# Optimization experiments

Hardware: AMD Instinct MI355X
Metric: run time of the kernel (lower is better)

Reference implementation:

```python
import jax, jax.numpy as jnp
import numpy as np
import math

B, S, D, H = 4, 2048, 2048, 16
HD = D // H  # 128


def _alibi_slopes(n_heads):
    # standard ALiBi slopes: 2^(-8/n * (h+1))
    return jnp.asarray([2.0 ** (-8.0 / n_heads * (h + 1)) for h in range(n_heads)], dtype=jnp.float32)


def setup_inputs() -> dict:
    key = jax.random.key(0)
    ks = jax.random.split(key, 10)
    w = lambda k: jax.random.normal(k, (D, D), dtype=jnp.float32) * 0.02
    b = lambda k: jax.random.normal(k, (D,), dtype=jnp.float32) * 0.01
    return {
        "hidden_states": jax.random.normal(ks[0], (B, S, D), dtype=jnp.float32),
        "Wq": w(ks[1]), "bq": b(ks[2]),
        "Wk": w(ks[3]), "bk": b(ks[4]),
        "Wv": w(ks[5]), "bv": b(ks[6]),
        "Wo": w(ks[7]), "bo": b(ks[8]),
        "alibi_slopes": _alibi_slopes(H),
    }


def reference(hidden_states, Wq, bq, Wk, bk, Wv, bv, Wo, bo, alibi_slopes):
    Bn, t, _ = hidden_states.shape
    split = lambda x: x.reshape(Bn, t, H, HD).transpose(0, 2, 1, 3)  # [B,H,S,hd]
    q = split(hidden_states @ Wq.T + bq)
    k = split(hidden_states @ Wk.T + bk)
    v = split(hidden_states @ Wv.T + bv)

    scores = jnp.einsum("bhsd,bhtd->bhst", q, k)  # [B,H,S,S]
    pos = jnp.arange(t)
    # alibi bias added BEFORE the 1/sqrt(hd) scaling, as in the torch code
    rel = (pos[None, :] - pos[:, None]).astype(scores.dtype)  # j - i
    bias = alibi_slopes[:, None, None] * rel  # [H,S,S]
    scores = (scores + bias[None]) / math.sqrt(HD)
    # grok-style tanh rescaling
    scores = 30.0 * jnp.tanh(scores / 30.0)
    causal = pos[:, None] >= pos[None, :]  # [S,S]
    scores = jnp.where(causal[None, None], scores, -jnp.inf)
    probs = jax.nn.softmax(scores, axis=-1)
    ctx = jnp.einsum("bhst,bhtd->bhsd", probs, v)
    ctx = ctx.transpose(0, 2, 1, 3).reshape(Bn, t, D)
    return ctx @ Wo.T + bo
```

## Files before the change

### kernel.cpp

```cpp
#include <hip/hip_runtime.h>

typedef unsigned int u32;
typedef unsigned short u16;
typedef __bf16 bf16x8 __attribute__((ext_vector_type(8)));
typedef float f32x4 __attribute__((ext_vector_type(4)));


__device__ __forceinline__ u16 f2bf(float f) {
  u32 u = __builtin_bit_cast(u32, f);
  u32 r = u + 0x7fffu + ((u >> 16) & 1u);
  return (u16)(r >> 16);
}

__device__ __forceinline__ void gload_lds16(const void* g, void* l) {
  __builtin_amdgcn_global_load_lds(
      (__attribute__((address_space(1))) void*)(g),
      (__attribute__((address_space(3))) void*)(l), 16, 0, 0);
}


__global__ __launch_bounds__(256) void convert_kernel(
    const float* __restrict__ hs, const float* __restrict__ wq,
    const float* __restrict__ wk, const float* __restrict__ wv,
    const float* __restrict__ wo,
    u16* __restrict__ hsb, u16* __restrict__ wqb, u16* __restrict__ wkb,
    u16* __restrict__ wvb, u16* __restrict__ wob) {
  long t = (long)blockIdx.x * 256 + threadIdx.x;
  const float* src;
  u16* dst;
  long off;
  if (t < 2097152) {
    src = hs; dst = hsb; off = t << 3;
  } else {
    long u = t - 2097152;
    int wi = (int)(u >> 19);
    off = (u & 524287) << 3;
    if (wi == 0)      { src = wq; dst = wqb; }
    else if (wi == 1) { src = wk; dst = wkb; }
    else if (wi == 2) { src = wv; dst = wvb; }
    else              { src = wo; dst = wob; }
  }
  float4 a = *(const float4*)(src + off);
  float4 b = *(const float4*)(src + off + 4);
  uint4 o;
  o.x = (u32)f2bf(a.x) | ((u32)f2bf(a.y) << 16);
  o.y = (u32)f2bf(a.z) | ((u32)f2bf(a.w) << 16);
  o.z = (u32)f2bf(b.x) | ((u32)f2bf(b.y) << 16);
  o.w = (u32)f2bf(b.z) | ((u32)f2bf(b.w) << 16);
  *(uint4*)(dst + off) = o;
}


template <int OF32>
__global__ __launch_bounds__(512, 2) void gemm256_kernel(
    const u16* __restrict__ A, const u16* __restrict__ Bw,
    const float* __restrict__ bias0, const float* __restrict__ bias1,
    const float* __restrict__ bias2, void* __restrict__ o0,
    void* __restrict__ o1, void* __restrict__ o2, int m_tiles, int n_tiles) {
  __shared__ __align__(16) char L[2][2][2][16384];

  const int tid = threadIdx.x;
  const int lane = tid & 63, w = tid >> 6;
  const int lr = lane & 15, lk = lane >> 4;
  const int wm = (w >> 2) * 128, wn = (w & 3) * 64;

  const int bid = blockIdx.x;
  const int xcd = bid & 7, loc = bid >> 3;
  const int npx = n_tiles >> 3;
  const int n_idx = xcd * npx + loc % npx;
  const int m_idx = loc / npx;
  const int m0 = m_idx * 256, n0 = n_idx * 256;

  const char* Ab = (const char*)A;
  const char* Bb = (const char*)Bw;
  const char* gA[2];
  const char* gB[2];
#pragma unroll
  for (int j = 0; j < 2; j++) {
    const int o = j * 8192 + tid * 16;
    const int row = o >> 6;
    const int c = (o & 63) ^ (((row >> 1) & 3) << 4);
    gA[j] = Ab + (size_t)(m0 + row) * 4096 + c;
    gB[j] = Bb + (size_t)(n0 + row) * 4096 + c;
  }

  auto stage = [&](int t, int kh, int isB) {
    char* Ld = &L[t & 1][isB][kh][0] + tid * 16;
    const int gof = t * 128 + kh * 64;
#pragma unroll
    for (int j = 0; j < 2; j++)
      gload_lds16((isB ? gB[j] : gA[j]) + gof, Ld + j * 8192);
  };
  auto rdA = [&](bf16x8* dst, int buf, int kh, int mset) {
#pragma unroll
    for (int m = 0; m < 4; m++) {
      const int row = wm + mset * 64 + m * 16 + lr;
      const int c = (lk * 16) ^ (((row >> 1) & 3) << 4);
      dst[m] = *(const bf16x8*)(&L[buf][0][kh][0] + row * 64 + c);
    }
  };
  auto rdB = [&](bf16x8* dst, int buf, int kh) {
#pragma unroll
    for (int n = 0; n < 4; n++) {
      const int row = wn + n * 16 + lr;
      const int c = (lk * 16) ^ (((row >> 1) & 3) << 4);
      dst[n] = *(const bf16x8*)(&L[buf][1][kh][0] + row * 64 + c);
    }
  };

  f32x4 acc[2][4][4];
#pragma unroll
  for (int s = 0; s < 2; s++)
#pragma unroll
    for (int m = 0; m < 4; m++)
#pragma unroll
      for (int n = 0; n < 4; n++) acc[s][m][n] = {0.f, 0.f, 0.f, 0.f};

  auto mm = [&](f32x4 (&ac)[4][4], bf16x8* a_, bf16x8* b_) {
    __builtin_amdgcn_s_setprio(1);
#pragma unroll
    for (int m = 0; m < 4; m++)
#pragma unroll
      for (int n = 0; n < 4; n++)
        ac[m][n] = __builtin_amdgcn_mfma_f32_16x16x32_bf16(a_[m], b_[n],
                                                           ac[m][n], 0, 0, 0);
    __builtin_amdgcn_s_setprio(0);
  };

  stage(0, 0, 0); stage(0, 0, 1); stage(0, 1, 0); stage(0, 1, 1);

  bf16x8 aP[4], aQ[4], b0[4], b1[4];
  for (int t = 0; t < 32; ++t) {
    const int buf = t & 1;
    const int t1 = (t + 1 < 32) ? t + 1 : 31;
    asm volatile("s_waitcnt vmcnt(4)" ::: "memory");
    asm volatile("s_barrier" ::: "memory");
    rdA(aP, buf, 0, 0);
    rdB(b0, buf, 0);
    stage(t1, 0, 0);
    if (t) mm(acc[1], aQ, b1);
    rdA(aQ, buf, 0, 1);
    stage(t1, 0, 1);
    mm(acc[0], aP, b0);
    asm volatile("s_waitcnt vmcnt(4)" ::: "memory");
    asm volatile("s_barrier" ::: "memory");
    rdA(aP, buf, 1, 0);
    rdB(b1, buf, 1);
    stage(t1, 1, 0);
    mm(acc[1], aQ, b0);
    rdA(aQ, buf, 1, 1);
    stage(t1, 1, 1);
    mm(acc[0], aP, b1);
  }
  mm(acc[1], aQ, b1);

  const float* bias;
  void* op;
  int nl0;
  if (OF32) {
    bias = bias0; op = o0; nl0 = n0;
  } else {
    const int seg = n0 >> 11;
    bias = seg == 0 ? bias0 : (seg == 1 ? bias1 : bias2);
    op = seg == 0 ? o0 : (seg == 1 ? o1 : o2);
    nl0 = n0 & 2047;
  }
#pragma unroll
  for (int n = 0; n < 4; n++) {
    const int col = nl0 + wn + n * 16 + lr;
    const float bv = bias[col];
#pragma unroll
    for (int s = 0; s < 2; s++)
#pragma unroll
      for (int m = 0; m < 4; m++) {
        const int grow = m0 + wm + s * 64 + m * 16 + lk * 4;
#pragma unroll
        for (int r = 0; r < 4; r++) {
          const float v = acc[s][m][n][r] + bv;
          if (OF32)
            ((float*)op)[(size_t)(grow + r) * 2048 + col] = v;
          else
            ((u16*)op)[(size_t)(grow + r) * 2048 + col] = f2bf(v);
        }
      }
  }
}


__global__ __launch_bounds__(512, 2) void attn_kernel(
    const u16* __restrict__ Qm, const u16* __restrict__ Km,
    const u16* __restrict__ Vm, const float* __restrict__ slopes,
    u16* __restrict__ ctx) {
  __shared__ __align__(16) char Ks[64 * 256];
  __shared__ __align__(16) char Vt[2][128 * 128];
  __shared__ __align__(16) char Pb[8][16 * 128];

  const int bid = blockIdx.x;
  const int sw = (bid & 7) * 64 + (bid >> 3);
  const int bh = sw >> 3, pi = sw & 7;
  const int b = bh >> 4, h = bh & 15;
  const int NTA = 2 * pi + 2;

  const int tid = threadIdx.x;
  const int lane = tid & 63, w = tid >> 6;
  const int lr = lane & 15, lk = lane >> 4;

  const char* Qb = (const char*)Qm + (size_t)b * 2048 * 4096 + h * 256;
  const char* Kb = (const char*)Km + (size_t)b * 2048 * 4096 + h * 256;
  const char* Vb = (const char*)Vm + (size_t)b * 2048 * 4096 + h * 256;

  const float SCALE = 0.08838834764831845f;
  const float sl_c = slopes[h] * SCALE;

  const float C1 = 1.4426950408889634f;
  const float C3 = -5.343315e-4f;
  const float C5 = 2.374806e-7f;
  const float C7 = -1.068005e-10f;

  float Tt[16];
#pragma unroll
  for (int nb = 0; nb < 4; nb++)
#pragma unroll
    for (int r = 0; r < 4; r++) Tt[nb * 4 + r] = sl_c * (float)(nb * 16 - r);

  const int vd0 = (tid & 15) * 8;
  const int vkv2 = tid >> 4;

  uint4 vr0, vr1;

  auto kvt_of = [&](int it) { return it < NTA ? it : it - NTA; };

  auto stageK = [&](int it) {
    const int kv0 = kvt_of(it) * 64;
#pragma unroll
    for (int j = 0; j < 2; j++) {
      const int o = j * 8192 + tid * 16;
      const int row = o >> 8, c = (o & 255) ^ ((row & 7) << 4);
      gload_lds16(Kb + (size_t)(kv0 + row) * 4096 + c, Ks + o);
    }
  };
  auto loadV = [&](int it) {
    const int kv0 = kvt_of(it) * 64;
    vr0 = *(const uint4*)(Vb + (size_t)(kv0 + vkv2 * 2) * 4096 + vd0 * 2);
    vr1 = *(const uint4*)(Vb + (size_t)(kv0 + vkv2 * 2 + 1) * 4096 + vd0 * 2);
  };
  auto writeV = [&](int bufi) {
    const u32* p0 = (const u32*)&vr0;
    const u32* p1 = (const u32*)&vr1;
#pragma unroll
    for (int wd = 0; wd < 4; wd++) {
      const u32 ev = __builtin_amdgcn_perm(p1[wd], p0[wd], 0x05040100u);
      const u32 od = __builtin_amdgcn_perm(p1[wd], p0[wd], 0x07060302u);
      const int d0_ = vd0 + 2 * wd, d1_ = d0_ + 1;
      *(u32*)(Vt[bufi] + d0_ * 128 +
              ((vkv2 * 4) ^ (((d0_ ^ (d0_ >> 3)) & 7) << 4))) = ev;
      *(u32*)(Vt[bufi] + d1_ * 128 +
              ((vkv2 * 4) ^ (((d1_ ^ (d1_ >> 3)) & 7) << 4))) = od;
    }
  };

  bf16x8 qf[4];
  f32x4 pv[8];
  float rs[4];
  int q0 = 0;

  stageK(0);
  loadV(0);

  for (int it = 0; it < 34; ++it) {
    const int bufi = it & 1;
    const int kv0 = kvt_of(it) * 64;

    if (it == 0 || it == NTA) {
      const int st = (it == 0) ? pi : (15 - pi);
      q0 = st * 128 + w * 16;
#pragma unroll
      for (int kc = 0; kc < 4; kc++)
        qf[kc] =
            *(const bf16x8*)(Qb + (size_t)(q0 + lr) * 4096 + kc * 64 + lk * 16);
#pragma unroll
      for (int i = 0; i < 8; i++) pv[i] = {0.f, 0.f, 0.f, 0.f};
      rs[0] = rs[1] = rs[2] = rs[3] = 0.f;
    }

    writeV(bufi);
    asm volatile("s_waitcnt vmcnt(0)" ::: "memory");
    __syncthreads();

    if (it + 1 < 34) loadV(it + 1);

    f32x4 sc[4];
    __builtin_amdgcn_s_setprio(1);
#pragma unroll
    for (int nb = 0; nb < 4; nb++) {
      f32x4 a = {0.f, 0.f, 0.f, 0.f};
      const int krow = nb * 16 + lr;
#pragma unroll
      for (int kc = 0; kc < 4; kc++) {
        const int off = krow * 256 + ((kc * 64 + lk * 16) ^ ((krow & 7) << 4));
        bf16x8 kf = *(const bf16x8*)(Ks + off);
        a = __builtin_amdgcn_mfma_f32_16x16x32_bf16(qf[kc], kf, a, 0, 0, 0);
      }
      sc[nb] = a;
    }
    __builtin_amdgcn_s_setprio(0);

    __syncthreads();
    if (it + 1 < 34) stageK(it + 1);

    const float aliB = sl_c * (float)(kv0 + lr - q0 - lk * 4);
#pragma unroll
    for (int nb = 0; nb < 4; nb++) {
      const int kv = kv0 + nb * 16 + lr;
#pragma unroll
      for (int r = 0; r < 4; r++) {
        const int q = q0 + lk * 4 + r;
        float z = fmaf(sc[nb][r], SCALE, aliB + Tt[nb * 4 + r]);
        z = fmaxf(-16.0f, fminf(z, 16.0f));
        const float u2 = z * z;
        float hh = fmaf(u2, C7, C5);
        hh = fmaf(u2, hh, C3);
        hh = fmaf(u2, hh, C1);
        float p = exp2f(z * hh);
        p = (kv <= q) ? p : 0.0f;
        rs[r] += p;
        const int qq = lk * 4 + r;
        const int off = qq * 128 + (((nb * 16 + lr) * 2) ^ ((qq & 7) << 4));
        const u32 ub = __builtin_bit_cast(u32, p);
        *(u16*)(Pb[w] + off) = (u16)((ub + 0x8000u) >> 16);
      }
    }

    __builtin_amdgcn_s_setprio(1);
#pragma unroll
    for (int kc = 0; kc < 2; kc++) {
      const int poff = lr * 128 + ((kc * 64 + lk * 16) ^ ((lr & 7) << 4));
      bf16x8 pf = *(const bf16x8*)(Pb[w] + poff);
#pragma unroll
      for (int db = 0; db < 8; db++) {
        const int d = db * 16 + lr;
        const int voff =
            d * 128 + ((kc * 64 + lk * 16) ^ (((d ^ (d >> 3)) & 7) << 4));
        bf16x8 vf = *(const bf16x8*)(Vt[bufi] + voff);
        pv[db] = __builtin_amdgcn_mfma_f32_16x16x32_bf16(pf, vf, pv[db], 0, 0, 0);
      }
    }
    __builtin_amdgcn_s_setprio(0);

    if (it == NTA - 1 || it == 33) {
      float inv[4];
#pragma unroll
      for (int r = 0; r < 4; r++) {
        float s = rs[r];
        s += __shfl_xor(s, 1);
        s += __shfl_xor(s, 2);
        s += __shfl_xor(s, 4);
        s += __shfl_xor(s, 8);
        inv[r] = 1.0f / s;
      }
      const size_t baserow = (size_t)b * 2048 + q0 + lk * 4;
#pragma unroll
      for (int db = 0; db < 8; db++)
#pragma unroll
        for (int r = 0; r < 4; r++)
          ctx[(baserow + r) * 2048 + h * 128 + db * 16 + lr] =
              f2bf(pv[db][r] * inv[r]);
    }
  }
}


extern "C" void kernel_launch(void* const* d_in, const int* in_sizes, int n_in,
                              void* d_out, int out_size, void* d_ws,
                              size_t ws_size, hipStream_t stream) {
  const float* hs = (const float*)d_in[0];
  const float* Wq = (const float*)d_in[1];
  const float* bq = (const float*)d_in[2];
  const float* Wk = (const float*)d_in[3];
  const float* bk = (const float*)d_in[4];
  const float* Wv = (const float*)d_in[5];
  const float* bv = (const float*)d_in[6];
  const float* Wo = (const float*)d_in[7];
  const float* bo = (const float*)d_in[8];
  const float* slopes = (const float*)d_in[9];

  char* ws = (char*)d_ws;
  u16* hsb = (u16*)(ws);
  u16* wqb = (u16*)(ws + 33554432);
  u16* wkb = (u16*)(ws + 41943040);
  u16* wvb = (u16*)(ws + 50331648);
  u16* wob = (u16*)(ws + 58720256);
  u16* Qb  = (u16*)(ws + 67108864);
  u16* Kb  = (u16*)(ws + 100663296);
  u16* Vb  = (u16*)(ws + 134217728);
  u16* ctxb = hsb;

  convert_kernel<<<16384, 256, 0, stream>>>(hs, Wq, Wk, Wv, Wo, hsb, wqb, wkb,
                                            wvb, wob);
  gemm256_kernel<0><<<768, 512, 0, stream>>>(hsb, wqb, bq, bk, bv, Qb, Kb, Vb,
                                             32, 24);
  attn_kernel<<<512, 512, 0, stream>>>(Qb, Kb, Vb, slopes, ctxb);
  gemm256_kernel<1><<<256, 512, 0, stream>>>(ctxb, wob, bo, bo, bo, d_out,
                                             d_out, d_out, 32, 8);
}
```

Before: 477.0 us.

## Double-buffer K tiles in LDS, single-buffer V, skip causal mask off-diagonal

Moves double buffering from the transposed V tile to the K tile, so the next K tile's global-to-LDS load is issued right after the barrier and overlaps the QK^T and softmax work of the current iteration. The barrier that sat between QK^T and the K staging is removed, and a new barrier is placed before the V write to protect the single V buffer. The per-element ALiBi bias precompute is folded into one register table plus a scalar, clamping uses med3, and the causal mask compare now runs only on diagonal tiles. The exchange is a different barrier placement and a changed LDS footprint, which could affect occupancy at two blocks per CU.

```diff
diff --git a/kernel.cpp b/kernel.cpp
--- a/kernel.cpp
+++ b/kernel.cpp
@@ -191,8 +191,8 @@
     const u16* __restrict__ Qm, const u16* __restrict__ Km,
     const u16* __restrict__ Vm, const float* __restrict__ slopes,
     u16* __restrict__ ctx) {
-  __shared__ __align__(16) char Ks[64 * 256];
-  __shared__ __align__(16) char Vt[2][128 * 128];
+  __shared__ __align__(16) char Ks[2][64 * 256];
+  __shared__ __align__(16) char Vt[128 * 128];
   __shared__ __align__(16) char Pb[8][16 * 128];
 
   const int bid = blockIdx.x;
@@ -217,11 +217,12 @@
   const float C5 = 2.374806e-7f;
   const float C7 = -1.068005e-10f;
 
-  float Tt[16];
+  float zo[16];
 #pragma unroll
   for (int nb = 0; nb < 4; nb++)
 #pragma unroll
-    for (int r = 0; r < 4; r++) Tt[nb * 4 + r] = sl_c * (float)(nb * 16 - r);
+    for (int r = 0; r < 4; r++)
+      zo[nb * 4 + r] = sl_c * (float)((lr - lk * 4) + nb * 16 - r);
 
   const int vd0 = (tid & 15) * 8;
   const int vkv2 = tid >> 4;
@@ -230,13 +231,13 @@
 
   auto kvt_of = [&](int it) { return it < NTA ? it : it - NTA; };
 
-  auto stageK = [&](int it) {
+  auto stageK = [&](int it, int buf) {
     const int kv0 = kvt_of(it) * 64;
 #pragma unroll
     for (int j = 0; j < 2; j++) {
       const int o = j * 8192 + tid * 16;
       const int row = o >> 8, c = (o & 255) ^ ((row & 7) << 4);
-      gload_lds16(Kb + (size_t)(kv0 + row) * 4096 + c, Ks + o);
+      gload_lds16(Kb + (size_t)(kv0 + row) * 4096 + c, Ks[buf] + o);
     }
   };
   auto loadV = [&](int it) {
@@ -244,7 +245,7 @@
     vr0 = *(const uint4*)(Vb + (size_t)(kv0 + vkv2 * 2) * 4096 + vd0 * 2);
     vr1 = *(const uint4*)(Vb + (size_t)(kv0 + vkv2 * 2 + 1) * 4096 + vd0 * 2);
   };
-  auto writeV = [&](int bufi) {
+  auto writeV = [&]() {
     const u32* p0 = (const u32*)&vr0;
     const u32* p1 = (const u32*)&vr1;
 #pragma unroll
@@ -252,9 +253,9 @@
       const u32 ev = __builtin_amdgcn_perm(p1[wd], p0[wd], 0x05040100u);
       const u32 od = __builtin_amdgcn_perm(p1[wd], p0[wd], 0x07060302u);
       const int d0_ = vd0 + 2 * wd, d1_ = d0_ + 1;
-      *(u32*)(Vt[bufi] + d0_ * 128 +
+      *(u32*)(Vt + d0_ * 128 +
               ((vkv2 * 4) ^ (((d0_ ^ (d0_ >> 3)) & 7) << 4))) = ev;
-      *(u32*)(Vt[bufi] + d1_ * 128 +
+      *(u32*)(Vt + d1_ * 128 +
               ((vkv2 * 4) ^ (((d1_ ^ (d1_ >> 3)) & 7) << 4))) = od;
     }
   };
@@ -264,11 +265,11 @@
   float rs[4];
   int q0 = 0;
 
-  stageK(0);
+  stageK(0, 0);
   loadV(0);
 
   for (int it = 0; it < 34; ++it) {
-    const int bufi = it & 1;
+    const int kb = it & 1;
     const int kv0 = kvt_of(it) * 64;
 
     if (it == 0 || it == NTA) {
@@ -283,11 +284,15 @@
       rs[0] = rs[1] = rs[2] = rs[3] = 0.f;
     }
 
-    writeV(bufi);
+    __syncthreads();
+    writeV();
     asm volatile("s_waitcnt vmcnt(0)" ::: "memory");
     __syncthreads();
 
-    if (it + 1 < 34) loadV(it + 1);
+    if (it + 1 < 34) {
+      stageK(it + 1, kb ^ 1);
+      loadV(it + 1);
+    }
 
     f32x4 sc[4];
     __builtin_amdgcn_s_setprio(1);
@@ -298,31 +303,31 @@
 #pragma unroll
       for (int kc = 0; kc < 4; kc++) {
         const int off = krow * 256 + ((kc * 64 + lk * 16) ^ ((krow & 7) << 4));
-        bf16x8 kf = *(const bf16x8*)(Ks + off);
+        bf16x8 kf = *(const bf16x8*)(Ks[kb] + off);
         a = __builtin_amdgcn_mfma_f32_16x16x32_bf16(qf[kc], kf, a, 0, 0, 0);
       }
       sc[nb] = a;
     }
     __builtin_amdgcn_s_setprio(0);
 
-    __syncthreads();
-    if (it + 1 < 34) stageK(it + 1);
-
-    const float aliB = sl_c * (float)(kv0 + lr - q0 - lk * 4);
+    const bool diag = (it < NTA) ? (it >= NTA - 2) : (it >= 32);
+    const float sb = sl_c * (float)(kv0 - q0);
 #pragma unroll
     for (int nb = 0; nb < 4; nb++) {
-      const int kv = kv0 + nb * 16 + lr;
 #pragma unroll
       for (int r = 0; r < 4; r++) {
-        const int q = q0 + lk * 4 + r;
-        float z = fmaf(sc[nb][r], SCALE, aliB + Tt[nb * 4 + r]);
-        z = fmaxf(-16.0f, fminf(z, 16.0f));
+        float z = fmaf(sc[nb][r], SCALE, zo[nb * 4 + r] + sb);
+        z = __builtin_amdgcn_fmed3f(z, -16.0f, 16.0f);
         const float u2 = z * z;
         float hh = fmaf(u2, C7, C5);
         hh = fmaf(u2, hh, C3);
         hh = fmaf(u2, hh, C1);
         float p = exp2f(z * hh);
-        p = (kv <= q) ? p : 0.0f;
+        if (diag) {
+          const int kv = kv0 + nb * 16 + lr;
+          const int q = q0 + lk * 4 + r;
+          p = (kv <= q) ? p : 0.0f;
+        }
         rs[r] += p;
         const int qq = lk * 4 + r;
         const int off = qq * 128 + (((nb * 16 + lr) * 2) ^ ((qq & 7) << 4));
@@ -341,7 +346,7 @@
         const int d = db * 16 + lr;
         const int voff =
             d * 128 + ((kc * 64 + lk * 16) ^ (((d ^ (d >> 3)) & 7) << 4));
-        bf16x8 vf = *(const bf16x8*)(Vt[bufi] + voff);
+        bf16x8 vf = *(const bf16x8*)(Vt + voff);
         pv[db] = __builtin_amdgcn_mfma_f32_16x16x32_bf16(pf, vf, pv[db], 0, 0, 0);
       }
     }
```

Measured after the change: 475.7 us. Within noise of the previous version (-0.3%).
